# Performance work log

Measured on AMD Instinct MI355X. Metric: run time of the kernel, lower is better.

## Reference

```python
import jax, jax.numpy as jnp
import numpy as np

TEMP = 0.5  # init kwarg `tmp`
NUM_CLASSES = 100


def setup_inputs() -> dict:
    key = jax.random.key(0)
    k1, k2 = jax.random.split(key)
    embedding = jax.random.normal(k1, (8192, 256), dtype=jnp.float32)
    label = jax.random.randint(k2, (8192,), 0, NUM_CLASSES, dtype=jnp.int64)
    return {"embedding": embedding, "label": label}


def reference(embedding, label):
    # Row-normalize -> pairwise cosine similarity [N, N]
    normed = embedding / jnp.linalg.norm(embedding, axis=1, keepdims=True)
    sim = (normed @ normed.T) / TEMP  # already divided by temperature

    N = embedding.shape[0]
    eye = jnp.eye(N, dtype=bool)

    # Denominator: sum of exp(sim) over off-diagonal entries per row
    exp_sim = jnp.exp(sim)
    row_sum = jnp.sum(jnp.where(eye, 0.0, exp_sim), axis=1)  # [N]

    # log(exp(sim_ij) / row_sum_i) = sim_ij - log(row_sum_i)
    log_prob = sim - jnp.log(row_sum)[:, None]

    # Positive mask: same label, i != j
    pos_mask = (label[:, None] == label[None, :]) & ~eye
    n_i = jnp.sum(pos_mask, axis=1)  # positives per anchor

    inner = jnp.sum(jnp.where(pos_mask, log_prob, 0.0), axis=1)  # [N]
    per_anchor = jnp.where(n_i > 0, -inner / jnp.maximum(n_i, 1).astype(sim.dtype), 0.0)
    return jnp.sum(per_anchor)
```

## Files before the change

### kernel.cpp

```cpp
#include <hip/hip_runtime.h>
#include <hip/hip_bf16.h>
#include <stdint.h>

#define N    8192
#define D    256
#define NCLS 100

static constexpr float TEMP    = 0.5f;
static constexpr float SCALE_F = 1.69864360f;
static constexpr float E2      = 7.38905609893065f;
static constexpr float LN2     = 0.69314718055994531f;

typedef __bf16 bf16x8 __attribute__((ext_vector_type(8)));
typedef float  f32x4  __attribute__((ext_vector_type(4)));

__device__ __forceinline__ unsigned short f2bf(float f) {
  union { float f; unsigned int u; } x; x.f = f;
  unsigned int r = x.u + 0x7fffu + ((x.u >> 16) & 1u);
  return (unsigned short)(r >> 16);
}
__device__ __forceinline__ float bf2f(unsigned short b) {
  union { unsigned int u; float f; } x; x.u = ((unsigned int)b) << 16;
  return x.f;
}
__device__ __forceinline__ void gld16(const void* g, void* l) {
  __builtin_amdgcn_global_load_lds(
      (const __attribute__((address_space(1))) unsigned int*)g,
      (__attribute__((address_space(3))) unsigned int*)l, 16, 0, 0);
}

__global__ __launch_bounds__(256) void normalize_kernel(
    const float* __restrict__ emb, const long long* __restrict__ label,
    unsigned short* __restrict__ abf, int* __restrict__ cnt,
    int* __restrict__ list) {
  const int row  = blockIdx.x * 4 + (threadIdx.x >> 6);
  const int lane = threadIdx.x & 63;
  const float4 v = ((const float4*)(emb + (size_t)row * D))[lane];
  float ss = v.x * v.x + v.y * v.y + v.z * v.z + v.w * v.w;
#pragma unroll
  for (int off = 1; off < 64; off <<= 1) ss += __shfl_xor(ss, off);
  const float s = rsqrtf(ss) * SCALE_F;
  ushort4 o;
  o.x = f2bf(v.x * s); o.y = f2bf(v.y * s);
  o.z = f2bf(v.z * s); o.w = f2bf(v.w * s);
  ((ushort4*)(abf + (size_t)row * D))[lane] = o;
  if (lane == 0) {
    const int c = (int)label[row];
    const int slot = atomicAdd(cnt + c, 1);
    list[c * 256 + slot] = row;
  }
}

#define TM 128
#define TN 128
#define BK 64
#define JT 4

__global__ __launch_bounds__(256) void simexp_rowsum_kernel(
    const unsigned short* __restrict__ A, float* __restrict__ rowsum) {
  __shared__ __align__(16) unsigned short sa[TM * BK];
  __shared__ __align__(16) unsigned short sb[TN * BK];
  const int tid  = threadIdx.x;
  const int w    = tid >> 6;
  const int lane = tid & 63;
  const int quad = lane >> 4;
  const int l15  = lane & 15;
  const int row0 = blockIdx.y * TM;
  const int jc0  = blockIdx.x * (TN * JT);
  const int wm   = (w & 1) * 64;
  const int wn   = (w >> 1) * 64;
  const int srow = lane >> 3;
  const int scol = (((lane & 7) ^ srow) << 3);

  float rowpart[4][4];
#pragma unroll
  for (int mt = 0; mt < 4; ++mt)
#pragma unroll
    for (int e = 0; e < 4; ++e) rowpart[mt][e] = 0.f;

  for (int jt = 0; jt < JT; ++jt) {
    const int jbase = jc0 + jt * TN;
    f32x4 acc[4][4];
#pragma unroll
    for (int mt = 0; mt < 4; ++mt)
#pragma unroll
      for (int nt = 0; nt < 4; ++nt) acc[mt][nt] = (f32x4){0.f, 0.f, 0.f, 0.f};

    for (int kc = 0; kc < D; kc += BK) {
#pragma unroll
      for (int p = 0; p < 4; ++p) {
        const int seg = p * 4 + w;
        const int r   = seg * 8 + srow;
        gld16(A + (size_t)(row0 + r) * D + kc + scol, sa + seg * 512);
        gld16(A + (size_t)(jbase + r) * D + kc + scol, sb + seg * 512);
      }
      __syncthreads();
#pragma unroll
      for (int kk = 0; kk < BK; kk += 32) {
        const int kb = (kk >> 3) + quad;
        const int sw = ((kb ^ (l15 & 7)) << 3);
        bf16x8 af[4], bfr[4];
#pragma unroll
        for (int mt = 0; mt < 4; ++mt)
          af[mt] = *(const bf16x8*)(sa + ((wm + mt * 16 + l15) << 6) + sw);
#pragma unroll
        for (int nt = 0; nt < 4; ++nt)
          bfr[nt] = *(const bf16x8*)(sb + ((wn + nt * 16 + l15) << 6) + sw);
#pragma unroll
        for (int mt = 0; mt < 4; ++mt)
#pragma unroll
          for (int nt = 0; nt < 4; ++nt)
            acc[mt][nt] = __builtin_amdgcn_mfma_f32_16x16x32_bf16(
                af[mt], bfr[nt], acc[mt][nt], 0, 0, 0);
      }
      __syncthreads();
    }
#pragma unroll
    for (int mt = 0; mt < 4; ++mt)
#pragma unroll
      for (int nt = 0; nt < 4; ++nt)
#pragma unroll
        for (int e = 0; e < 4; ++e)
          rowpart[mt][e] += __builtin_amdgcn_exp2f(acc[mt][nt][e]);
  }
#pragma unroll
  for (int mt = 0; mt < 4; ++mt)
#pragma unroll
    for (int e = 0; e < 4; ++e) {
      float v = rowpart[mt][e];
      v += __shfl_xor(v, 1);
      v += __shfl_xor(v, 2);
      v += __shfl_xor(v, 4);
      v += __shfl_xor(v, 8);
      if (l15 == 0)
        atomicAdd(&rowsum[row0 + wm + mt * 16 + quad * 4 + e], v);
    }
}

__global__ __launch_bounds__(256) void finalize_kernel(
    const unsigned short* __restrict__ abf, const float* __restrict__ rowsum,
    const long long* __restrict__ label, const int* __restrict__ cnt,
    const int* __restrict__ list, float* __restrict__ out) {
  __shared__ float red[4];
  __shared__ int rows_l[256];
  const int tid  = threadIdx.x;
  const int w    = tid >> 6;
  const int lane = tid & 63;

  if (blockIdx.x < NCLS) {
    const int c = blockIdx.x;
    const int m = cnt[c];
    if (m <= 1) return;
    if (tid < m) rows_l[tid] = list[c * 256 + tid];
    __syncthreads();
    float acc = 0.f;
    for (int s = 0; s < m; ++s)
      acc += bf2f(abf[(size_t)rows_l[s] * D + tid]);
    float v = acc * acc;
#pragma unroll
    for (int off = 1; off < 64; off <<= 1) v += __shfl_xor(v, off);
    if (lane == 0) red[w] = v;
    __syncthreads();
    if (tid == 0) {
      const float ssq = red[0] + red[1] + red[2] + red[3];
      const float term = (ssq * LN2 - 2.0f * (float)m) / (float)(m - 1);
      atomicAdd(out, -term);
    }
  } else {
    const int i = (blockIdx.x - NCLS) * 256 + tid;
    const int c = (int)label[i];
    float v = 0.f;
    if (cnt[c] > 1)
      v = __builtin_amdgcn_logf(rowsum[i] - E2) * LN2;
#pragma unroll
    for (int off = 1; off < 64; off <<= 1) v += __shfl_xor(v, off);
    if (lane == 0) red[w] = v;
    __syncthreads();
    if (tid == 0)
      atomicAdd(out, red[0] + red[1] + red[2] + red[3]);
  }
}

extern "C" void kernel_launch(void* const* d_in, const int* in_sizes, int n_in,
                              void* d_out, int out_size, void* d_ws,
                              size_t ws_size, hipStream_t stream) {
  const float* emb = (const float*)d_in[0];
  const long long* label = (const long long*)d_in[1];
  float* out = (float*)d_out;

  char* ws = (char*)d_ws;
  unsigned short* abf = (unsigned short*)ws;
  float* rowsum = (float*)(ws + (size_t)N * D * 2);
  int* cnt = (int*)(rowsum + N);
  int* list = cnt + 128;

  hipMemsetAsync(rowsum, 0, (size_t)N * 4 + 128 * 4, stream);
  hipMemsetAsync(out, 0, sizeof(float), stream);

  normalize_kernel<<<N / 4, 256, 0, stream>>>(emb, label, abf, cnt, list);
  dim3 gridB(N / (TN * JT), N / TM);
  simexp_rowsum_kernel<<<gridB, 256, 0, stream>>>(abf, rowsum);
  finalize_kernel<<<NCLS + N / 256, 256, 0, stream>>>(abf, rowsum, label, cnt,
                                                      list, out);
}
```

Before: 134.6 us.

## Exploit similarity matrix symmetry by computing only upper-triangular tiles

The sim-exp-rowsum kernel now launches a triangular grid that covers only the tile pairs with column block at or above the row block. Each off-diagonal tile adds its exp values to the row sums and also to the column sums through extra shuffles and atomics, so roughly half the GEMM and exp work is skipped. In exchange it adds a per-block loop to map the linear block index to a tile pair, more atomics on rowsum, and some load imbalance from skipped sub-tiles inside blocks.

```diff
diff --git a/kernel.cpp b/kernel.cpp
--- a/kernel.cpp
+++ b/kernel.cpp
@@ -54,7 +54,12 @@
 #define TM 128
 #define TN 128
 #define BK 64
-#define JT 4
+#define JT 2
+
+__device__ __forceinline__ int tri_off(int bi) {
+  const int q = bi >> 1, r = bi & 1;
+  return 32 * bi - q * (q - 1 + r);
+}
 
 __global__ __launch_bounds__(256) void simexp_rowsum_kernel(
     const unsigned short* __restrict__ A, float* __restrict__ rowsum) {
@@ -65,8 +70,16 @@
   const int lane = tid & 63;
   const int quad = lane >> 4;
   const int l15  = lane & 15;
-  const int row0 = blockIdx.y * TM;
-  const int jc0  = blockIdx.x * (TN * JT);
+
+  int bi = 0;
+  {
+    const int id = blockIdx.x;
+    while (bi < 63 && tri_off(bi + 1) <= id) ++bi;
+  }
+  const int sj   = (bi >> 1) + (blockIdx.x - tri_off(bi));
+  const int row0 = bi * TM;
+  const int jc0  = sj * (TN * JT);
+
   const int wm   = (w & 1) * 64;
   const int wn   = (w >> 1) * 64;
   const int srow = lane >> 3;
@@ -80,6 +93,9 @@
 
   for (int jt = 0; jt < JT; ++jt) {
     const int jbase = jc0 + jt * TN;
+    if (jbase < row0) continue;
+    const bool diag = (jbase == row0);
+
     f32x4 acc[4][4];
 #pragma unroll
     for (int mt = 0; mt < 4; ++mt)
@@ -115,14 +131,30 @@
       }
       __syncthreads();
     }
+
+    float cs[4] = {0.f, 0.f, 0.f, 0.f};
 #pragma unroll
     for (int mt = 0; mt < 4; ++mt)
 #pragma unroll
       for (int nt = 0; nt < 4; ++nt)
 #pragma unroll
-        for (int e = 0; e < 4; ++e)
-          rowpart[mt][e] += __builtin_amdgcn_exp2f(acc[mt][nt][e]);
-  }
+        for (int e = 0; e < 4; ++e) {
+          const float v = __builtin_amdgcn_exp2f(acc[mt][nt][e]);
+          rowpart[mt][e] += v;
+          cs[nt] += v;
+        }
+    if (!diag) {
+#pragma unroll
+      for (int nt = 0; nt < 4; ++nt) {
+        float v = cs[nt];
+        v += __shfl_xor(v, 16);
+        v += __shfl_xor(v, 32);
+        if (lane < 16)
+          atomicAdd(&rowsum[jbase + wn + nt * 16 + lane], v);
+      }
+    }
+  }
+
 #pragma unroll
   for (int mt = 0; mt < 4; ++mt)
 #pragma unroll
@@ -198,8 +230,9 @@
   hipMemsetAsync(out, 0, sizeof(float), stream);
 
   normalize_kernel<<<N / 4, 256, 0, stream>>>(emb, label, abf, cnt, list);
-  dim3 gridB(N / (TN * JT), N / TM);
-  simexp_rowsum_kernel<<<gridB, 256, 0, stream>>>(abf, rowsum);
+
+  simexp_rowsum_kernel<<<1056, 256, 0, stream>>>(abf, rowsum);
+
   finalize_kernel<<<NCLS + N / 256, 256, 0, stream>>>(abf, rowsum, label, cnt,
                                                       list, out);
 }
```

Result: no change. 134.0 us (-0.4%).

## Exploit similarity symmetry with triangular tile grid and 32x32 MFMA

Applied to the files above, without the earlier changes.

The sim-exp-rowsum kernel now launches only the upper-triangular 128x128 tile pairs (2080 blocks). Each off-diagonal tile contributes both row sums and column sums, which roughly halves the GEMM and exp work of the symmetric similarity matrix. The MFMA shape moves from 16x16x32 to 32x32x16 with a 2x2 accumulator layout, and the launch bounds request 4 blocks per CU. The trade-offs are more atomics per tile for the column sums, the loss of the per-block JT reuse of the A tile, and an integer/sqrt index decode per block.

```diff
diff --git a/kernel.cpp b/kernel.cpp
--- a/kernel.cpp
+++ b/kernel.cpp
@@ -12,7 +12,7 @@
 static constexpr float LN2     = 0.69314718055994531f;
 
 typedef __bf16 bf16x8 __attribute__((ext_vector_type(8)));
-typedef float  f32x4  __attribute__((ext_vector_type(4)));
+typedef float  f32x16 __attribute__((ext_vector_type(16)));
 
 __device__ __forceinline__ unsigned short f2bf(float f) {
   union { float f; unsigned int u; } x; x.f = f;
@@ -52,89 +52,105 @@
 }
 
 #define TM 128
-#define TN 128
 #define BK 64
-#define JT 4
-
-__global__ __launch_bounds__(256) void simexp_rowsum_kernel(
+
+__global__ __launch_bounds__(256, 4) void simexp_rowsum_kernel(
     const unsigned short* __restrict__ A, float* __restrict__ rowsum) {
   __shared__ __align__(16) unsigned short sa[TM * BK];
-  __shared__ __align__(16) unsigned short sb[TN * BK];
+  __shared__ __align__(16) unsigned short sb[TM * BK];
   const int tid  = threadIdx.x;
   const int w    = tid >> 6;
   const int lane = tid & 63;
-  const int quad = lane >> 4;
-  const int l15  = lane & 15;
-  const int row0 = blockIdx.y * TM;
-  const int jc0  = blockIdx.x * (TN * JT);
+  const int l31  = lane & 31;
+  const int half = lane >> 5;
+
+  const int id = blockIdx.x;
+  int bi = (int)((129.0f - sqrtf(16641.0f - 8.0f * (float)id)) * 0.5f);
+  while (bi > 0 && (bi * (129 - bi)) / 2 > id) --bi;
+  while (((bi + 1) * (128 - bi)) / 2 <= id) ++bi;
+  const int bj   = bi + (id - (bi * (129 - bi)) / 2);
+  const int row0 = bi * TM;
+  const int jb0  = bj * TM;
+  const bool diag = (bi == bj);
+
   const int wm   = (w & 1) * 64;
   const int wn   = (w >> 1) * 64;
   const int srow = lane >> 3;
   const int scol = (((lane & 7) ^ srow) << 3);
 
-  float rowpart[4][4];
-#pragma unroll
-  for (int mt = 0; mt < 4; ++mt)
-#pragma unroll
-    for (int e = 0; e < 4; ++e) rowpart[mt][e] = 0.f;
-
-  for (int jt = 0; jt < JT; ++jt) {
-    const int jbase = jc0 + jt * TN;
-    f32x4 acc[4][4];
-#pragma unroll
-    for (int mt = 0; mt < 4; ++mt)
-#pragma unroll
-      for (int nt = 0; nt < 4; ++nt) acc[mt][nt] = (f32x4){0.f, 0.f, 0.f, 0.f};
-
-    for (int kc = 0; kc < D; kc += BK) {
-#pragma unroll
-      for (int p = 0; p < 4; ++p) {
-        const int seg = p * 4 + w;
-        const int r   = seg * 8 + srow;
-        gld16(A + (size_t)(row0 + r) * D + kc + scol, sa + seg * 512);
-        gld16(A + (size_t)(jbase + r) * D + kc + scol, sb + seg * 512);
+  f32x16 acc[2][2];
+#pragma unroll
+  for (int mt = 0; mt < 2; ++mt)
+#pragma unroll
+    for (int nt = 0; nt < 2; ++nt)
+#pragma unroll
+      for (int r = 0; r < 16; ++r) acc[mt][nt][r] = 0.f;
+
+  for (int kc = 0; kc < D; kc += BK) {
+#pragma unroll
+    for (int p = 0; p < 4; ++p) {
+      const int seg = p * 4 + w;
+      const int r   = seg * 8 + srow;
+      gld16(A + (size_t)(row0 + r) * D + kc + scol, sa + seg * 512);
+      gld16(A + (size_t)(jb0 + r) * D + kc + scol, sb + seg * 512);
+    }
+    __syncthreads();
+#pragma unroll
+    for (int ks = 0; ks < 4; ++ks) {
+      const int kb = ks * 2 + half;
+      const int sw = ((kb ^ (l31 & 7)) << 3);
+      bf16x8 af[2], bfr[2];
+#pragma unroll
+      for (int mt = 0; mt < 2; ++mt)
+        af[mt] = *(const bf16x8*)(sa + ((wm + mt * 32 + l31) << 6) + sw);
+#pragma unroll
+      for (int nt = 0; nt < 2; ++nt)
+        bfr[nt] = *(const bf16x8*)(sb + ((wn + nt * 32 + l31) << 6) + sw);
+#pragma unroll
+      for (int mt = 0; mt < 2; ++mt)
+#pragma unroll
+        for (int nt = 0; nt < 2; ++nt)
+          acc[mt][nt] = __builtin_amdgcn_mfma_f32_32x32x16_bf16(
+              af[mt], bfr[nt], acc[mt][nt], 0, 0, 0);
+    }
+    __syncthreads();
+  }
+
+  float cs[2] = {0.f, 0.f};
+#pragma unroll
+  for (int mt = 0; mt < 2; ++mt) {
+    float rp[16];
+#pragma unroll
+    for (int nt = 0; nt < 2; ++nt)
+#pragma unroll
+      for (int r = 0; r < 16; ++r) {
+        const float v = __builtin_amdgcn_exp2f(acc[mt][nt][r]);
+        if (nt == 0) rp[r] = v; else rp[r] += v;
+        cs[nt] += v;
       }
-      __syncthreads();
-#pragma unroll
-      for (int kk = 0; kk < BK; kk += 32) {
-        const int kb = (kk >> 3) + quad;
-        const int sw = ((kb ^ (l15 & 7)) << 3);
-        bf16x8 af[4], bfr[4];
-#pragma unroll
-        for (int mt = 0; mt < 4; ++mt)
-          af[mt] = *(const bf16x8*)(sa + ((wm + mt * 16 + l15) << 6) + sw);
-#pragma unroll
-        for (int nt = 0; nt < 4; ++nt)
-          bfr[nt] = *(const bf16x8*)(sb + ((wn + nt * 16 + l15) << 6) + sw);
-#pragma unroll
-        for (int mt = 0; mt < 4; ++mt)
-#pragma unroll
-          for (int nt = 0; nt < 4; ++nt)
-            acc[mt][nt] = __builtin_amdgcn_mfma_f32_16x16x32_bf16(
-                af[mt], bfr[nt], acc[mt][nt], 0, 0, 0);
-      }
-      __syncthreads();
-    }
-#pragma unroll
-    for (int mt = 0; mt < 4; ++mt)
-#pragma unroll
-      for (int nt = 0; nt < 4; ++nt)
-#pragma unroll
-        for (int e = 0; e < 4; ++e)
-          rowpart[mt][e] += __builtin_amdgcn_exp2f(acc[mt][nt][e]);
-  }
-#pragma unroll
-  for (int mt = 0; mt < 4; ++mt)
-#pragma unroll
-    for (int e = 0; e < 4; ++e) {
-      float v = rowpart[mt][e];
+#pragma unroll
+    for (int r = 0; r < 16; ++r) {
+      float v = rp[r];
       v += __shfl_xor(v, 1);
       v += __shfl_xor(v, 2);
       v += __shfl_xor(v, 4);
       v += __shfl_xor(v, 8);
-      if (l15 == 0)
-        atomicAdd(&rowsum[row0 + wm + mt * 16 + quad * 4 + e], v);
-    }
+      v += __shfl_xor(v, 16);
+      if (l31 == 0)
+        atomicAdd(&rowsum[row0 + wm + mt * 32 + (r & 3) + 8 * (r >> 2) +
+                          4 * half],
+                  v);
+    }
+  }
+  if (!diag) {
+#pragma unroll
+    for (int nt = 0; nt < 2; ++nt) {
+      float v = cs[nt];
+      v += __shfl_xor(v, 32);
+      if (half == 0)
+        atomicAdd(&rowsum[jb0 + wn + nt * 32 + l31], v);
+    }
+  }
 }
 
 __global__ __launch_bounds__(256) void finalize_kernel(
@@ -198,8 +214,9 @@
   hipMemsetAsync(out, 0, sizeof(float), stream);
 
   normalize_kernel<<<N / 4, 256, 0, stream>>>(emb, label, abf, cnt, list);
-  dim3 gridB(N / (TN * JT), N / TM);
-  simexp_rowsum_kernel<<<gridB, 256, 0, stream>>>(abf, rowsum);
+
+  simexp_rowsum_kernel<<<2080, 256, 0, stream>>>(abf, rowsum);
+
   finalize_kernel<<<NCLS + N / 256, 256, 0, stream>>>(abf, rowsum, label, cnt,
                                                       list, out);
 }
```

Measured after the change: 156.7 us. 1.16x slower.

## Compute similarity GEMM in FP8 MFMA instead of BF16

Applied to the files above, without the earlier changes.

The normalize kernel now also writes an FP8 copy of the scaled normalized embeddings. The sim-exp row-sum GEMM loads these FP8 rows into LDS with a new XOR swizzle and uses the 16x16x32 FP8 MFMA. The finalize kernel still uses the BF16 copy. This halves the bytes loaded per tile and uses the higher-rate FP8 matrix path, at the cost of more rounding error in the exp row sums.

```diff
diff --git a/kernel.cpp b/kernel.cpp
--- a/kernel.cpp
+++ b/kernel.cpp
@@ -11,8 +11,7 @@
 static constexpr float E2      = 7.38905609893065f;
 static constexpr float LN2     = 0.69314718055994531f;
 
-typedef __bf16 bf16x8 __attribute__((ext_vector_type(8)));
-typedef float  f32x4  __attribute__((ext_vector_type(4)));
+typedef float f32x4 __attribute__((ext_vector_type(4)));
 
 __device__ __forceinline__ unsigned short f2bf(float f) {
   union { float f; unsigned int u; } x; x.f = f;
@@ -31,8 +30,8 @@
 
 __global__ __launch_bounds__(256) void normalize_kernel(
     const float* __restrict__ emb, const long long* __restrict__ label,
-    unsigned short* __restrict__ abf, int* __restrict__ cnt,
-    int* __restrict__ list) {
+    unsigned short* __restrict__ abf, unsigned char* __restrict__ a8,
+    int* __restrict__ cnt, int* __restrict__ list) {
   const int row  = blockIdx.x * 4 + (threadIdx.x >> 6);
   const int lane = threadIdx.x & 63;
   const float4 v = ((const float4*)(emb + (size_t)row * D))[lane];
@@ -40,10 +39,16 @@
 #pragma unroll
   for (int off = 1; off < 64; off <<= 1) ss += __shfl_xor(ss, off);
   const float s = rsqrtf(ss) * SCALE_F;
+  const float x = v.x * s, y = v.y * s, z = v.z * s, wv = v.w * s;
+
   ushort4 o;
-  o.x = f2bf(v.x * s); o.y = f2bf(v.y * s);
-  o.z = f2bf(v.z * s); o.w = f2bf(v.w * s);
+  o.x = f2bf(x); o.y = f2bf(y); o.z = f2bf(z); o.w = f2bf(wv);
   ((ushort4*)(abf + (size_t)row * D))[lane] = o;
+
+  int p = __builtin_amdgcn_cvt_pk_fp8_f32(x, y, 0, false);
+  p = __builtin_amdgcn_cvt_pk_fp8_f32(z, wv, p, true);
+  ((int*)(a8 + (size_t)row * D))[lane] = p;
+
   if (lane == 0) {
     const int c = (int)label[row];
     const int slot = atomicAdd(cnt + c, 1);
@@ -53,13 +58,13 @@
 
 #define TM 128
 #define TN 128
-#define BK 64
+#define BKB 128
 #define JT 4
 
 __global__ __launch_bounds__(256) void simexp_rowsum_kernel(
-    const unsigned short* __restrict__ A, float* __restrict__ rowsum) {
-  __shared__ __align__(16) unsigned short sa[TM * BK];
-  __shared__ __align__(16) unsigned short sb[TN * BK];
+    const unsigned char* __restrict__ A, float* __restrict__ rowsum) {
+  __shared__ __align__(16) unsigned char sa[TM * BKB];
+  __shared__ __align__(16) unsigned char sb[TN * BKB];
   const int tid  = threadIdx.x;
   const int w    = tid >> 6;
   const int lane = tid & 63;
@@ -70,7 +75,7 @@
   const int wm   = (w & 1) * 64;
   const int wn   = (w >> 1) * 64;
   const int srow = lane >> 3;
-  const int scol = (((lane & 7) ^ srow) << 3);
+  const int sblk = lane & 7;
 
   float rowpart[4][4];
 #pragma unroll
@@ -86,35 +91,43 @@
 #pragma unroll
       for (int nt = 0; nt < 4; ++nt) acc[mt][nt] = (f32x4){0.f, 0.f, 0.f, 0.f};
 
-    for (int kc = 0; kc < D; kc += BK) {
+    for (int kc = 0; kc < D; kc += BKB) {
 #pragma unroll
       for (int p = 0; p < 4; ++p) {
         const int seg = p * 4 + w;
         const int r   = seg * 8 + srow;
-        gld16(A + (size_t)(row0 + r) * D + kc + scol, sa + seg * 512);
-        gld16(A + (size_t)(jbase + r) * D + kc + scol, sb + seg * 512);
+        const int sc  = kc + ((sblk ^ ((r >> 1) & 7)) << 4);
+        gld16(A + (size_t)(row0 + r) * D + sc, sa + seg * 1024);
+        gld16(A + (size_t)(jbase + r) * D + sc, sb + seg * 1024);
       }
       __syncthreads();
 #pragma unroll
-      for (int kk = 0; kk < BK; kk += 32) {
-        const int kb = (kk >> 3) + quad;
-        const int sw = ((kb ^ (l15 & 7)) << 3);
-        bf16x8 af[4], bfr[4];
+      for (int kk = 0; kk < 4; ++kk) {
+        const int b16 = kk * 2 + (quad >> 1);
+        const int s8  = (quad & 1) * 8;
+        long af[4], bf[4];
+#pragma unroll
+        for (int mt = 0; mt < 4; ++mt) {
+          const int m = wm + mt * 16 + l15;
+          af[mt] = *(const long*)(sa + m * BKB +
+                                  ((b16 ^ ((m >> 1) & 7)) << 4) + s8);
+        }
+#pragma unroll
+        for (int nt = 0; nt < 4; ++nt) {
+          const int n = wn + nt * 16 + l15;
+          bf[nt] = *(const long*)(sb + n * BKB +
+                                  ((b16 ^ ((n >> 1) & 7)) << 4) + s8);
+        }
 #pragma unroll
         for (int mt = 0; mt < 4; ++mt)
-          af[mt] = *(const bf16x8*)(sa + ((wm + mt * 16 + l15) << 6) + sw);
-#pragma unroll
-        for (int nt = 0; nt < 4; ++nt)
-          bfr[nt] = *(const bf16x8*)(sb + ((wn + nt * 16 + l15) << 6) + sw);
-#pragma unroll
-        for (int mt = 0; mt < 4; ++mt)
 #pragma unroll
           for (int nt = 0; nt < 4; ++nt)
-            acc[mt][nt] = __builtin_amdgcn_mfma_f32_16x16x32_bf16(
-                af[mt], bfr[nt], acc[mt][nt], 0, 0, 0);
+            acc[mt][nt] = __builtin_amdgcn_mfma_f32_16x16x32_fp8_fp8(
+                af[mt], bf[nt], acc[mt][nt], 0, 0, 0);
       }
       __syncthreads();
     }
+
 #pragma unroll
     for (int mt = 0; mt < 4; ++mt)
 #pragma unroll
@@ -123,6 +136,7 @@
         for (int e = 0; e < 4; ++e)
           rowpart[mt][e] += __builtin_amdgcn_exp2f(acc[mt][nt][e]);
   }
+
 #pragma unroll
   for (int mt = 0; mt < 4; ++mt)
 #pragma unroll
@@ -190,16 +204,19 @@
 
   char* ws = (char*)d_ws;
   unsigned short* abf = (unsigned short*)ws;
-  float* rowsum = (float*)(ws + (size_t)N * D * 2);
+  unsigned char* a8 = (unsigned char*)(ws + (size_t)N * D * 2);
+  float* rowsum = (float*)(ws + (size_t)N * D * 3);
   int* cnt = (int*)(rowsum + N);
   int* list = cnt + 128;
 
   hipMemsetAsync(rowsum, 0, (size_t)N * 4 + 128 * 4, stream);
   hipMemsetAsync(out, 0, sizeof(float), stream);
 
-  normalize_kernel<<<N / 4, 256, 0, stream>>>(emb, label, abf, cnt, list);
+  normalize_kernel<<<N / 4, 256, 0, stream>>>(emb, label, abf, a8, cnt, list);
+
   dim3 gridB(N / (TN * JT), N / TM);
-  simexp_rowsum_kernel<<<gridB, 256, 0, stream>>>(abf, rowsum);
+  simexp_rowsum_kernel<<<gridB, 256, 0, stream>>>(a8, rowsum);
+
   finalize_kernel<<<NCLS + N / 256, 256, 0, stream>>>(abf, rowsum, label, cnt,
                                                       list, out);
 }
```

New measurement: 133.4 us. No clear change (-0.9%).
